# Kernel optimization log

Measured on AMD Instinct MI355X. Metric: run time of the kernel, lower is better.

## Reference

```python
import jax, jax.numpy as jnp
import numpy as np

D_INP=36; D_MODEL=144; NHEAD=4; NHID=128; NLAYERS=2
MAX_LEN=215; D_STATIC=9; D_PE=16; N_CLASSES=2; B=128
D_OB=D_MODEL//D_INP; GCH=MAX_LEN*D_OB; D_TR=D_MODEL+D_PE; D_FINAL=D_TR+D_INP
_EI=np.stack(np.nonzero(np.ones((D_INP,D_INP),dtype=np.int64)))  # torch.nonzero(ones).T -> all pairs
SRC_N=jnp.asarray(_EI[0]); TGT_N=jnp.asarray(_EI[1]); N_EDGE=_EI.shape[1]


def setup_inputs():
    ks=jax.random.split(jax.random.key(0),40)
    def w(i,shape,s=0.05): return jax.random.normal(ks[i],shape,jnp.float32)*s
    return {
      'src': jax.random.normal(ks[0],(MAX_LEN,B,2*D_INP),jnp.float32),
      'static': jax.random.normal(ks[1],(B,D_STATIC),jnp.float32),
      'times': jax.random.uniform(ks[2],(MAX_LEN,B),jnp.float32)*MAX_LEN,
      'lengths': jax.random.randint(ks[3],(B,),32,MAX_LEN+1),
      'R_u': w(4,(1,D_INP*D_OB)),
      'emb_w': w(5,(D_INP,D_STATIC)), 'emb_b': jnp.zeros(D_INP,jnp.float32),
      'Wv1': w(6,(GCH,GCH),1.0/np.sqrt(GCH)), 'bv1': jnp.zeros(GCH,jnp.float32),
      'Wv2': w(7,(GCH,GCH),1.0/np.sqrt(GCH)), 'bv2': jnp.zeros(GCH,jnp.float32),
      'in_proj_w': w(8,(NLAYERS,3*D_TR,D_TR)), 'in_proj_b': jnp.zeros((NLAYERS,3*D_TR),jnp.float32),
      'out_w': w(9,(NLAYERS,D_TR,D_TR)), 'out_b': jnp.zeros((NLAYERS,D_TR),jnp.float32),
      'lin1_w': w(10,(NLAYERS,NHID,D_TR)), 'lin1_b': jnp.zeros((NLAYERS,NHID),jnp.float32),
      'lin2_w': w(11,(NLAYERS,D_TR,NHID)), 'lin2_b': jnp.zeros((NLAYERS,D_TR),jnp.float32),
      'ln1_s': jnp.ones((NLAYERS,D_TR),jnp.float32), 'ln1_b': jnp.zeros((NLAYERS,D_TR),jnp.float32),
      'ln2_s': jnp.ones((NLAYERS,D_TR),jnp.float32), 'ln2_b': jnp.zeros((NLAYERS,D_TR),jnp.float32),
      'mlp1_w': w(12,(D_FINAL,D_FINAL)), 'mlp1_b': jnp.zeros(D_FINAL,jnp.float32),
      'mlp2_w': w(13,(N_CLASSES,D_FINAL)), 'mlp2_b': jnp.zeros(N_CLASSES,jnp.float32),
    }


def _seg_softmax(wgt, seg, n):
    m=jnp.full((n,),-jnp.inf,wgt.dtype).at[seg].max(wgt)
    e=jnp.exp(wgt-m[seg])
    s=jnp.zeros((n,),wgt.dtype).at[seg].add(e)
    return e/s[seg]


def _ln(x,s,b):
    mu=jnp.mean(x,-1,keepdims=True); v=jnp.var(x,-1,keepdims=True)
    return (x-mu)/jnp.sqrt(v+1e-5)*s+b


def _forward(src, static, times, R_u, emb_w, emb_b, Wv1, bv1, Wv2, bv2, in_proj_w, in_proj_b, out_w, out_b, lin1_w, lin1_b, lin2_w, lin2_b, ln1_s, ln1_b, ln2_s, ln2_b, mlp1_w, mlp1_b, mlp2_w, mlp2_b, lengths):
    T,Bb=src.shape[0],src.shape[1]
    obs=src[:,:,:D_INP]                                  # drop mask half
    h=jax.nn.relu(jnp.repeat(obs,D_OB,axis=-1)*R_u)      # h_u = relu(x_u*R_u), [T,B,144]
    ts=jnp.asarray(MAX_LEN**np.linspace(0,1,D_PE//2),jnp.float32)
    scaled=times[:,:,None]/ts
    pe=jnp.concatenate([jnp.sin(scaled),jnp.cos(scaled)],-1)  # [T,B,16]
    emb=static@emb_w.T+emb_b                             # [B,36]
    # --- Observation_progation x2 (use_beta=False): gather-softmax-scatter per sensor graph ---
    xb=h.transpose(1,0,2).reshape(Bb,T,D_INP,D_OB).transpose(0,2,1,3).reshape(Bb,D_INP,GCH)
    ew=jnp.ones((N_EDGE,),jnp.float32)                   # adj=ones -> edge_weights=1
    gamma=_seg_softmax(ew,TGT_N,D_INP)                   # softmax over edges per target node
    def prop(x_,Wv,bv):
        V=jax.nn.relu(x_@Wv.T+bv)                        # relu(lin_value(x_j))
        msgs=V[:,SRC_N,:]*gamma[None,:,None]             # gather source features per edge
        return jnp.zeros_like(x_).at[:,TGT_N,:].add(msgs)  # scatter-add to targets
    x1=prop(xb,Wv1,bv1)
    x2=prop(x1,Wv2,bv2)                                  # layer2 uses alpha1 = raw edge_weights
    alpha=jnp.broadcast_to(ew[None,:],(Bb,N_EDGE))       # alpha_all.T
    sq=jnp.sum(alpha*alpha,1)
    d2=jnp.maximum(sq[:,None]+sq[None,:]-2.0*(alpha@alpha.T),0.0)
    distance=jnp.mean(jnp.sqrt(d2))
    out=x2.reshape(Bb,D_INP,T,D_OB).transpose(2,0,1,3).reshape(T,Bb,D_INP*D_OB)
    x=jnp.concatenate([out,pe],-1)                       # [T,B,160]
    mask=jnp.arange(T)[None,:]>=lengths[:,None]          # [B,T] True = padded
    hd=D_TR//NHEAD
    for l in range(NLAYERS):                             # torch post-norm TransformerEncoderLayer
        qkv=x@in_proj_w[l].T+in_proj_b[l]
        q,k,v=jnp.split(qkv,3,-1)
        def heads(t): return t.reshape(T,Bb,NHEAD,hd).transpose(1,2,0,3)  # [B,H,T,hd]
        sc=jnp.einsum('bhqd,bhkd->bhqk',heads(q),heads(k))/np.sqrt(hd)
        sc=jnp.where(mask[:,None,None,:],jnp.float32(-1e30),sc)
        o=jnp.einsum('bhqk,bhkd->bhqd',jax.nn.softmax(sc,-1),heads(v))
        o=o.transpose(2,0,1,3).reshape(T,Bb,D_TR)@out_w[l].T+out_b[l]
        x=_ln(x+o,ln1_s[l],ln1_b[l])
        ff=jax.nn.relu(x@lin1_w[l].T+lin1_b[l])@lin2_w[l].T+lin2_b[l]
        x=_ln(x+ff,ln2_s[l],ln2_b[l])
    valid=1.0-mask.T[:,:,None].astype(x.dtype)           # [T,B,1]
    agg=jnp.sum(x*valid,0)/(lengths[:,None].astype(x.dtype)+1.0)
    feat=jnp.concatenate([agg,emb],1)                    # [B,196]
    logits=jax.nn.relu(feat@mlp1_w.T+mlp1_b)@mlp2_w.T+mlp2_b
    return logits,distance


def reference(src, static, times, lengths, R_u, emb_w, emb_b, Wv1, bv1, Wv2, bv2, in_proj_w, in_proj_b, out_w, out_b, lin1_w, lin1_b, lin2_w, lin2_b, ln1_s, ln1_b, ln2_s, ln2_b, mlp1_w, mlp1_b, mlp2_w, mlp2_b):
    return _forward(src, static, times, R_u, emb_w, emb_b, Wv1, bv1, Wv2, bv2, in_proj_w, in_proj_b, out_w, out_b, lin1_w, lin1_b, lin2_w, lin2_b, ln1_s, ln1_b, ln2_s, ln2_b, mlp1_w, mlp1_b, mlp2_w, mlp2_b, lengths)
```

## Files before the change

kernel.cpp:

```cpp
#include <hip/hip_runtime.h>
#include <math.h>

#define T_LEN 215
#define TP    224
#define B_N   128
#define DINP  36
#define D_TR  160
#define HD    40
#define D_FIN 196
#define KPG   864

typedef __attribute__((ext_vector_type(8))) short short8v;
typedef __attribute__((ext_vector_type(4))) float f32x4;

__device__ __forceinline__ ushort f2bf(float x) {
  union { float f; unsigned u; } c; c.f = x;
  unsigned r = c.u + 0x7fffu + ((c.u >> 16) & 1u);
  return (ushort)(r >> 16);
}
__device__ __forceinline__ float bf2f(ushort h) {
  union { unsigned u; float f; } c; c.u = ((unsigned)h) << 16;
  return c.f;
}

__global__ __launch_bounds__(256) void k_prep(const float* __restrict__ Wv1,
    const float* __restrict__ Wv2, const float* __restrict__ ipw, const float* __restrict__ ow,
    const float* __restrict__ l1w, const float* __restrict__ l2w,
    const float* __restrict__ src, const float* __restrict__ R_u,
    const float* __restrict__ stat, const float* __restrict__ emb_w, const float* __restrict__ emb_b,
    ushort* __restrict__ wv1b, ushort* __restrict__ wv2b, ushort* __restrict__ ipwb,
    ushort* __restrict__ owb, ushort* __restrict__ l1wb, ushort* __restrict__ l2wb,
    float* __restrict__ v2acc, float* __restrict__ featacc,
    ushort* __restrict__ obuf16, ushort* __restrict__ xb16) {
  __shared__ float Ss[T_LEN * DINP];
  if (blockIdx.x >= 8202) {
    const int b = blockIdx.x - 8202, tid = threadIdx.x;
    for (int i = tid; i < T_LEN * DINP; i += 256) {
      int t = i / DINP, j = i - t * DINP;
      Ss[i] = src[((size_t)t * B_N + b) * 72 + j];
    }
    __syncthreads();
    for (int i = tid; i < DINP * T_LEN; i += 256) {
      int ii = i / T_LEN, t = i - ii * T_LEN;
      float v = Ss[t * DINP + ii];
      float4 r = ((const float4*)R_u)[ii];
      ushort4 o;
      o.x = f2bf(fmaxf(v * r.x, 0.f)); o.y = f2bf(fmaxf(v * r.y, 0.f));
      o.z = f2bf(fmaxf(v * r.z, 0.f)); o.w = f2bf(fmaxf(v * r.w, 0.f));
      ushort* row = xb16 + (size_t)(b * DINP + ii) * KPG;
      *(ushort4*)(row + 4 * t) = o;
      if (t == 0) { ushort4 z = {0, 0, 0, 0}; *(ushort4*)(row + 860) = z; }
    }
    return;
  }
  int i = blockIdx.x * 256 + threadIdx.x;
  if (i < 746496) { int n = i / KPG, k = i % KPG;
    wv1b[i] = (n < 860 && k < 860) ? f2bf(Wv1[n * 860 + k]) : (ushort)0; return; }
  i -= 746496;
  if (i < 746496) { int n = i / KPG, k = i % KPG;
    wv2b[i] = (n < 860 && k < 860) ? f2bf(Wv2[n * 860 + k]) : (ushort)0; return; }
  i -= 746496;
  if (i < 153600) { ipwb[i] = f2bf(ipw[i]); return; }
  i -= 153600;
  if (i < 51200)  { owb[i] = f2bf(ow[i]); return; }
  i -= 51200;
  if (i < 40960)  { l1wb[i] = f2bf(l1w[i]); return; }
  i -= 40960;
  if (i < 40960)  { l2wb[i] = f2bf(l2w[i]); return; }
  i -= 40960;
  if (i < 110592) { v2acc[i] = 0.f; return; }
  i -= 110592;
  if (i < 20480)  { int b = i / D_TR, d = i - b * D_TR;
    featacc[b * D_FIN + d] = 0.f; return; }
  i -= 20480;
  if (i < 4608)   { int b = i / DINP, ii = i - b * DINP;
    float s = emb_b[ii];
    #pragma unroll
    for (int k = 0; k < 9; k++) s = fmaf(stat[b * 9 + k], emb_w[ii * 9 + k], s);
    featacc[b * D_FIN + D_TR + ii] = s; return; }
  i -= 4608;
  if (i < 184320) {
    int b = i / 1440, rem = i % 1440;
    int t = 215 + rem / 160, cc = rem % 160;
    obuf16[((size_t)b * TP + t) * D_TR + cc] = 0; return;
  }
}

__global__ __launch_bounds__(256) void k_red_s1(const ushort* __restrict__ V1b, ushort* __restrict__ s1) {
  int idx = blockIdx.x * 256 + threadIdx.x;
  if (idx >= B_N * KPG) return;
  int b = idx / KPG, n = idx % KPG;
  float s = 0.f;
  if (n < 860) {
    #pragma unroll 4
    for (int i = 0; i < DINP; i++) s += bf2f(V1b[((size_t)b * DINP + i) * 860 + n]);
    s *= (1.0f / 36.0f);
  }
  s1[idx] = (n < 860) ? f2bf(s) : (ushort)0;
}

__global__ __launch_bounds__(256) void k_buildx(const float* __restrict__ v2acc,
    const float* __restrict__ bv2, const float* __restrict__ times,
    ushort* __restrict__ x16) {
  int idx = blockIdx.x * 256 + threadIdx.x;
  if (idx >= B_N * TP * 40) return;
  int c = idx % 40;
  int r = idx / 40;
  int t = r % TP, b = r / TP;
  float4 f = {0.f, 0.f, 0.f, 0.f};
  if (t < T_LEN) {
    if (c < 36) {
      float4 a = *(const float4*)&v2acc[(size_t)b * KPG + 4 * t];
      float4 bb = *(const float4*)&bv2[4 * t];
      f.x = fmaxf(a.x + bb.x, 0.f); f.y = fmaxf(a.y + bb.y, 0.f);
      f.z = fmaxf(a.z + bb.z, 0.f); f.w = fmaxf(a.w + bb.w, 0.f);
    } else {
      float tm = times[t * B_N + b];
      int j0 = (c - 36) * 4;
      bool is_sin = j0 < 8;
      int kb = j0 & 7;
      float o[4];
      #pragma unroll
      for (int qq = 0; qq < 4; qq++) {
        float ts = expf((float)(kb + qq) * 0.76723400f);
        float sc = tm / ts;
        o[qq] = is_sin ? sinf(sc) : cosf(sc);
      }
      f.x = o[0]; f.y = o[1]; f.z = o[2]; f.w = o[3];
    }
  }
  ushort4 h = {f2bf(f.x), f2bf(f.y), f2bf(f.z), f2bf(f.w)};
  *(ushort4*)(x16 + (size_t)r * D_TR + 4 * c) = h;
}

template <int RELU, int SPLIT, int WMODE, int BNT>
__global__ __launch_bounds__(256) void gemm_bf16(const ushort* __restrict__ A,
    const ushort* __restrict__ W, const float* __restrict__ bias, void* __restrict__ Cv,
    int KP, int ldc, int ncols, int kts) {
  __shared__ ushort As[128 * 32];
  __shared__ ushort Ws[BNT * 32];
  constexpr int NJ = BNT / 16;
  const int tid = threadIdx.x;
  const int wave = tid >> 6, lane = tid & 63;
  const int lr = lane & 15, hi = lane >> 4;
  const int m0 = blockIdx.y * 128, n0 = blockIdx.x * BNT;
  const int kt0 = blockIdx.z * kts;

  f32x4 acc[2][NJ];
  #pragma unroll
  for (int i = 0; i < 2; i++)
    #pragma unroll
    for (int j = 0; j < NJ; j++) acc[i][j] = (f32x4){0.f, 0.f, 0.f, 0.f};

  const int ar = tid >> 2, g = tid & 3;
  const size_t abase0 = (size_t)(m0 + ar) * KP;
  const size_t abase1 = (size_t)(m0 + ar + 64) * KP;
  const size_t bbase0 = (size_t)(n0 + ar) * KP;
  const size_t bbase1 = (size_t)(n0 + ar + 64) * KP;
  const int awb0 = ar * 64 + ((g * 16) ^ ((ar & 3) << 4));
  const int awb1 = awb0 + 64 * 64;

  const int arow0 = wave * 32 + lr;
  const int arb0 = arow0 * 64 + ((hi * 16) ^ ((arow0 & 3) << 4));
  const int arb1 = (arow0 + 16) * 64 + ((hi * 16) ^ (((arow0 + 16) & 3) << 4));
  int brb[NJ];
  #pragma unroll
  for (int j = 0; j < NJ; j++)
    brb[j] = (j * 16 + lr) * 64 + ((hi * 16) ^ ((lr & 3) << 4));

  for (int kt = 0; kt < kts; ++kt) {
    const int k0 = (kt0 + kt) * 32;
    uint4 va0 = *(const uint4*)(A + abase0 + k0 + g * 8);
    uint4 va1 = *(const uint4*)(A + abase1 + k0 + g * 8);
    uint4 vb0 = *(const uint4*)(W + bbase0 + k0 + g * 8);
    uint4 vb1;
    if constexpr (BNT == 128) vb1 = *(const uint4*)(W + bbase1 + k0 + g * 8);
    if (kt) __syncthreads();
    *(uint4*)((char*)As + awb0) = va0;
    *(uint4*)((char*)As + awb1) = va1;
    *(uint4*)((char*)Ws + awb0) = vb0;
    if constexpr (BNT == 128) *(uint4*)((char*)Ws + awb1) = vb1;
    __syncthreads();
    short8v a0 = *(const short8v*)((const char*)As + arb0);
    short8v a1 = *(const short8v*)((const char*)As + arb1);
    #pragma unroll
    for (int j = 0; j < NJ; j++) {
      short8v bf = *(const short8v*)((const char*)Ws + brb[j]);
      acc[0][j] = __builtin_amdgcn_mfma_f32_16x16x32_bf16(a0, bf, acc[0][j], 0, 0, 0);
      acc[1][j] = __builtin_amdgcn_mfma_f32_16x16x32_bf16(a1, bf, acc[1][j], 0, 0, 0);
    }
  }

  #pragma unroll
  for (int i = 0; i < 2; i++) {
    #pragma unroll
    for (int j = 0; j < NJ; j++) {
      int col = n0 + j * 16 + lr;
      int row = m0 + wave * 32 + i * 16 + hi * 4;
      if (col < ncols) {
        if constexpr (SPLIT) {
          #pragma unroll
          for (int r = 0; r < 4; r++)
            atomicAdd((float*)Cv + (size_t)(row + r) * ldc + col, acc[i][j][r]);
        } else {
          float bb = bias ? bias[col] : 0.f;
          #pragma unroll
          for (int r = 0; r < 4; r++) {
            float xv = acc[i][j][r] + bb;
            if (RELU) xv = fmaxf(xv, 0.f);
            if (WMODE == 0) ((float*)Cv)[(size_t)(row + r) * ldc + col] = xv;
            else            ((ushort*)Cv)[(size_t)(row + r) * ldc + col] = f2bf(xv);
          }
        }
      }
    }
  }
}

__global__ __launch_bounds__(256) void gemm_qkv(const ushort* __restrict__ A,
    const ushort* __restrict__ W, const float* __restrict__ bias,
    ushort* __restrict__ qkvB, ushort* __restrict__ Vt, int kts) {
  __shared__ ushort As[128 * 32];
  __shared__ ushort Ws[128 * 32];
  const int KP = 160;
  const int tid = threadIdx.x;
  const int wave = tid >> 6, lane = tid & 63;
  const int lr = lane & 15, hi = lane >> 4;
  const int m0 = blockIdx.y * 128, n0 = blockIdx.x * 128;

  f32x4 acc[2][8];
  #pragma unroll
  for (int i = 0; i < 2; i++)
    #pragma unroll
    for (int j = 0; j < 8; j++) acc[i][j] = (f32x4){0.f, 0.f, 0.f, 0.f};

  const int ar = tid >> 2, g = tid & 3;
  const size_t abase0 = (size_t)(m0 + ar) * KP;
  const size_t abase1 = (size_t)(m0 + ar + 64) * KP;
  const size_t bbase0 = (size_t)(n0 + ar) * KP;
  const size_t bbase1 = (size_t)(n0 + ar + 64) * KP;
  const int awb0 = ar * 64 + ((g * 16) ^ ((ar & 3) << 4));
  const int awb1 = awb0 + 64 * 64;

  const int arow0 = wave * 32 + lr;
  const int arb0 = arow0 * 64 + ((hi * 16) ^ ((arow0 & 3) << 4));
  const int arb1 = (arow0 + 16) * 64 + ((hi * 16) ^ (((arow0 + 16) & 3) << 4));
  int brb[8];
  #pragma unroll
  for (int j = 0; j < 8; j++)
    brb[j] = (j * 16 + lr) * 64 + ((hi * 16) ^ ((lr & 3) << 4));

  for (int kt = 0; kt < kts; ++kt) {
    const int k0 = kt * 32;
    uint4 va0 = *(const uint4*)(A + abase0 + k0 + g * 8);
    uint4 va1 = *(const uint4*)(A + abase1 + k0 + g * 8);
    uint4 vb0 = *(const uint4*)(W + bbase0 + k0 + g * 8);
    uint4 vb1 = *(const uint4*)(W + bbase1 + k0 + g * 8);
    if (kt) __syncthreads();
    *(uint4*)((char*)As + awb0) = va0;
    *(uint4*)((char*)As + awb1) = va1;
    *(uint4*)((char*)Ws + awb0) = vb0;
    *(uint4*)((char*)Ws + awb1) = vb1;
    __syncthreads();
    short8v a0 = *(const short8v*)((const char*)As + arb0);
    short8v a1 = *(const short8v*)((const char*)As + arb1);
    #pragma unroll
    for (int j = 0; j < 8; j++) {
      short8v bf = *(const short8v*)((const char*)Ws + brb[j]);
      acc[0][j] = __builtin_amdgcn_mfma_f32_16x16x32_bf16(a0, bf, acc[0][j], 0, 0, 0);
      acc[1][j] = __builtin_amdgcn_mfma_f32_16x16x32_bf16(a1, bf, acc[1][j], 0, 0, 0);
    }
  }

  #pragma unroll
  for (int i = 0; i < 2; i++) {
    const int row = m0 + wave * 32 + i * 16 + hi * 4;
    const int b = row / TP, t0 = row - b * TP;
    #pragma unroll
    for (int j = 0; j < 8; j++) {
      int col = n0 + j * 16 + lr;
      if (col < 320) {
        float bb = bias[col];
        #pragma unroll
        for (int r = 0; r < 4; r++)
          qkvB[(size_t)(row + r) * 480 + col] = f2bf(acc[i][j][r] + bb);
      } else if (col < 480) {
        float bb = bias[col];
        int dg = col - 320;
        int hh = dg / 40, dd = dg - hh * 40;
        ushort4 pv;
        pv.x = f2bf(acc[i][j][0] + bb); pv.y = f2bf(acc[i][j][1] + bb);
        pv.z = f2bf(acc[i][j][2] + bb); pv.w = f2bf(acc[i][j][3] + bb);
        *(ushort4*)(Vt + (((size_t)(b * 4 + hh) * 48 + dd) * TP + t0)) = pv;
      }
    }
  }
}

__global__ __launch_bounds__(256) void gemm_ln(const ushort* __restrict__ A,
    const ushort* __restrict__ W, const float* __restrict__ bias,
    const float* __restrict__ gam, const float* __restrict__ bet,
    ushort* __restrict__ x16, int KP, int kts,
    const int* __restrict__ lengths, float* __restrict__ featacc) {
  __shared__ ushort As[64 * 32];
  __shared__ ushort Ws[160 * 32];
  const int tid = threadIdx.x;
  const int wave = tid >> 6, lane = tid & 63;
  const int lr = lane & 15, hi = lane >> 4;
  const int m0 = blockIdx.x * 64;

  f32x4 acc[10];
  #pragma unroll
  for (int j = 0; j < 10; j++) acc[j] = (f32x4){0.f, 0.f, 0.f, 0.f};

  const int ar = tid >> 2, g = tid & 3;
  const size_t abase = (size_t)(m0 + ar) * KP;
  const int awb = ar * 64 + ((g * 16) ^ ((ar & 3) << 4));
  const int wr0 = tid >> 2,         ws0 = tid & 3;
  const int wr1 = (tid + 256) >> 2, ws1 = (tid + 256) & 3;
  const int wr2 = (tid + 512) >> 2, ws2 = (tid + 512) & 3;
  const int wwb0 = wr0 * 64 + ((ws0 * 16) ^ ((wr0 & 3) << 4));
  const int wwb1 = wr1 * 64 + ((ws1 * 16) ^ ((wr1 & 3) << 4));
  const int wwb2 = wr2 * 64 + ((ws2 * 16) ^ ((wr2 & 3) << 4));

  const int arow = wave * 16 + lr;
  const int arb = arow * 64 + ((hi * 16) ^ ((arow & 3) << 4));
  int brb[10];
  #pragma unroll
  for (int j = 0; j < 10; j++)
    brb[j] = (j * 16 + lr) * 64 + ((hi * 16) ^ ((lr & 3) << 4));

  for (int kt = 0; kt < kts; ++kt) {
    const int k0 = kt * 32;
    uint4 va = *(const uint4*)(A + abase + k0 + g * 8);
    uint4 w0 = *(const uint4*)(W + (size_t)wr0 * KP + k0 + ws0 * 8);
    uint4 w1 = *(const uint4*)(W + (size_t)wr1 * KP + k0 + ws1 * 8);
    uint4 w2;
    if (tid < 128) w2 = *(const uint4*)(W + (size_t)wr2 * KP + k0 + ws2 * 8);
    if (kt) __syncthreads();
    *(uint4*)((char*)As + awb) = va;
    *(uint4*)((char*)Ws + wwb0) = w0;
    *(uint4*)((char*)Ws + wwb1) = w1;
    if (tid < 128) *(uint4*)((char*)Ws + wwb2) = w2;
    __syncthreads();
    short8v a0 = *(const short8v*)((const char*)As + arb);
    #pragma unroll
    for (int j = 0; j < 10; j++) {
      short8v bf = *(const short8v*)((const char*)Ws + brb[j]);
      acc[j] = __builtin_amdgcn_mfma_f32_16x16x32_bf16(a0, bf, acc[j], 0, 0, 0);
    }
  }

  const int rb = m0 + wave * 16 + hi * 4;
  float s[4] = {0.f, 0.f, 0.f, 0.f};
  #pragma unroll
  for (int j = 0; j < 10; j++) {
    const int col = j * 16 + lr;
    const float bb = bias[col];
    #pragma unroll
    for (int r = 0; r < 4; r++) {
      float v = acc[j][r] + bb + bf2f(x16[(size_t)(rb + r) * D_TR + col]);
      acc[j][r] = v;
      s[r] += v;
    }
  }
  #pragma unroll
  for (int r = 0; r < 4; r++) {
    s[r] += __shfl_xor(s[r], 1, 64);
    s[r] += __shfl_xor(s[r], 2, 64);
    s[r] += __shfl_xor(s[r], 4, 64);
    s[r] += __shfl_xor(s[r], 8, 64);
  }
  float mu[4], q2[4] = {0.f, 0.f, 0.f, 0.f};
  #pragma unroll
  for (int r = 0; r < 4; r++) mu[r] = s[r] * (1.0f / 160.0f);
  #pragma unroll
  for (int j = 0; j < 10; j++)
    #pragma unroll
    for (int r = 0; r < 4; r++) {
      float d = acc[j][r] - mu[r];
      q2[r] += d * d;
    }
  #pragma unroll
  for (int r = 0; r < 4; r++) {
    q2[r] += __shfl_xor(q2[r], 1, 64);
    q2[r] += __shfl_xor(q2[r], 2, 64);
    q2[r] += __shfl_xor(q2[r], 4, 64);
    q2[r] += __shfl_xor(q2[r], 8, 64);
  }
  float rstd[4];
  #pragma unroll
  for (int r = 0; r < 4; r++) rstd[r] = rsqrtf(q2[r] * (1.0f / 160.0f) + 1e-5f);

  if (featacc == nullptr) {
    #pragma unroll
    for (int j = 0; j < 10; j++) {
      const int col = j * 16 + lr;
      const float gc = gam[col], bc = bet[col];
      #pragma unroll
      for (int r = 0; r < 4; r++) {
        float o = (acc[j][r] - mu[r]) * rstd[r] * gc + bc;
        x16[(size_t)(rb + r) * D_TR + col] = f2bf(o);
      }
    }
  } else {
    const int b = rb / TP, t0 = rb - b * TP;
    int L = lengths[b]; if (L > T_LEN) L = T_LEN;
    #pragma unroll
    for (int j = 0; j < 10; j++) {
      const int col = j * 16 + lr;
      const float gc = gam[col], bc = bet[col];
      float sacc = 0.f;
      #pragma unroll
      for (int r = 0; r < 4; r++) {
        float o = (acc[j][r] - mu[r]) * rstd[r] * gc + bc;
        if (t0 + r < L) sacc += o;
      }
      if (t0 < L) atomicAdd(&featacc[b * D_FIN + col], sacc);
    }
  }
}

__global__ __launch_bounds__(256) void gemm_ff(const ushort* __restrict__ x16in,
    const ushort* __restrict__ W1, const float* __restrict__ b1,
    const ushort* __restrict__ W2, const float* __restrict__ b2,
    const float* __restrict__ gam, const float* __restrict__ bet,
    ushort* __restrict__ x16, const int* __restrict__ lengths,
    float* __restrict__ featacc) {
  __shared__ ushort As[64 * 32];
  __shared__ ushort W1s[128 * 32];
  __shared__ ushort W2s[160 * 32];
  __shared__ ushort Hs[64 * 136];
  const int tid = threadIdx.x;
  const int wave = tid >> 6, lane = tid & 63;
  const int lr = lane & 15, hi = lane >> 4;
  const int m0 = blockIdx.x * 64;

  f32x4 acc1[8];
  #pragma unroll
  for (int j = 0; j < 8; j++) acc1[j] = (f32x4){0.f, 0.f, 0.f, 0.f};

  const int ar = tid >> 2, g = tid & 3;
  const size_t abase = (size_t)(m0 + ar) * 160;
  const int awb = ar * 64 + ((g * 16) ^ ((ar & 3) << 4));
  const int awb1 = awb + 64 * 64;
  const size_t w1base0 = (size_t)ar * 160;
  const size_t w1base1 = (size_t)(ar + 64) * 160;

  const int arow = wave * 16 + lr;
  const int arb = arow * 64 + ((hi * 16) ^ ((arow & 3) << 4));
  int brb8[8];
  #pragma unroll
  for (int j = 0; j < 8; j++)
    brb8[j] = (j * 16 + lr) * 64 + ((hi * 16) ^ ((lr & 3) << 4));

  for (int kt = 0; kt < 5; ++kt) {
    const int k0 = kt * 32;
    uint4 va  = *(const uint4*)(x16in + abase + k0 + g * 8);
    uint4 w10 = *(const uint4*)(W1 + w1base0 + k0 + g * 8);
    uint4 w11 = *(const uint4*)(W1 + w1base1 + k0 + g * 8);
    if (kt) __syncthreads();
    *(uint4*)((char*)As + awb) = va;
    *(uint4*)((char*)W1s + awb) = w10;
    *(uint4*)((char*)W1s + awb1) = w11;
    __syncthreads();
    short8v a0 = *(const short8v*)((const char*)As + arb);
    #pragma unroll
    for (int j = 0; j < 8; j++) {
      short8v bf = *(const short8v*)((const char*)W1s + brb8[j]);
      acc1[j] = __builtin_amdgcn_mfma_f32_16x16x32_bf16(a0, bf, acc1[j], 0, 0, 0);
    }
  }
  {
    const int rr = wave * 16 + hi * 4;
    #pragma unroll
    for (int j = 0; j < 8; j++) {
      const int col = j * 16 + lr;
      const float bb = b1[col];
      #pragma unroll
      for (int r = 0; r < 4; r++)
        Hs[(rr + r) * 136 + col] = f2bf(fmaxf(acc1[j][r] + bb, 0.f));
    }
  }
  __syncthreads();

  f32x4 acc[10];
  #pragma unroll
  for (int j = 0; j < 10; j++) acc[j] = (f32x4){0.f, 0.f, 0.f, 0.f};

  const int wr0 = tid >> 2,         ws0 = tid & 3;
  const int wr1 = (tid + 256) >> 2, ws1 = (tid + 256) & 3;
  const int wr2 = (tid + 512) >> 2, ws2 = (tid + 512) & 3;
  const int wwb0 = wr0 * 64 + ((ws0 * 16) ^ ((wr0 & 3) << 4));
  const int wwb1 = wr1 * 64 + ((ws1 * 16) ^ ((wr1 & 3) << 4));
  const int wwb2 = wr2 * 64 + ((ws2 * 16) ^ ((wr2 & 3) << 4));
  int brb[10];
  #pragma unroll
  for (int j = 0; j < 10; j++)
    brb[j] = (j * 16 + lr) * 64 + ((hi * 16) ^ ((lr & 3) << 4));

  for (int kt = 0; kt < 4; ++kt) {
    const int k0 = kt * 32;
    uint4 w0 = *(const uint4*)(W2 + (size_t)wr0 * 128 + k0 + ws0 * 8);
    uint4 w1 = *(const uint4*)(W2 + (size_t)wr1 * 128 + k0 + ws1 * 8);
    uint4 w2;
    if (tid < 128) w2 = *(const uint4*)(W2 + (size_t)wr2 * 128 + k0 + ws2 * 8);
    if (kt) __syncthreads();
    *(uint4*)((char*)W2s + wwb0) = w0;
    *(uint4*)((char*)W2s + wwb1) = w1;
    if (tid < 128) *(uint4*)((char*)W2s + wwb2) = w2;
    __syncthreads();
    short8v a0 = *(const short8v*)(&Hs[(wave * 16 + lr) * 136 + k0 + hi * 8]);
    #pragma unroll
    for (int j = 0; j < 10; j++) {
      short8v bf = *(const short8v*)((const char*)W2s + brb[j]);
      acc[j] = __builtin_amdgcn_mfma_f32_16x16x32_bf16(a0, bf, acc[j], 0, 0, 0);
    }
  }

  const int rb = m0 + wave * 16 + hi * 4;
  float s[4] = {0.f, 0.f, 0.f, 0.f};
  #pragma unroll
  for (int j = 0; j < 10; j++) {
    const int col = j * 16 + lr;
    const float bb = b2[col];
    #pragma unroll
    for (int r = 0; r < 4; r++) {
      float v = acc[j][r] + bb + bf2f(x16[(size_t)(rb + r) * D_TR + col]);
      acc[j][r] = v;
      s[r] += v;
    }
  }
  #pragma unroll
  for (int r = 0; r < 4; r++) {
    s[r] += __shfl_xor(s[r], 1, 64);
    s[r] += __shfl_xor(s[r], 2, 64);
    s[r] += __shfl_xor(s[r], 4, 64);
    s[r] += __shfl_xor(s[r], 8, 64);
  }
  float mu[4], q2[4] = {0.f, 0.f, 0.f, 0.f};
  #pragma unroll
  for (int r = 0; r < 4; r++) mu[r] = s[r] * (1.0f / 160.0f);
  #pragma unroll
  for (int j = 0; j < 10; j++)
    #pragma unroll
    for (int r = 0; r < 4; r++) {
      float d = acc[j][r] - mu[r];
      q2[r] += d * d;
    }
  #pragma unroll
  for (int r = 0; r < 4; r++) {
    q2[r] += __shfl_xor(q2[r], 1, 64);
    q2[r] += __shfl_xor(q2[r], 2, 64);
    q2[r] += __shfl_xor(q2[r], 4, 64);
    q2[r] += __shfl_xor(q2[r], 8, 64);
  }
  float rstd[4];
  #pragma unroll
  for (int r = 0; r < 4; r++) rstd[r] = rsqrtf(q2[r] * (1.0f / 160.0f) + 1e-5f);

  if (featacc == nullptr) {
    #pragma unroll
    for (int j = 0; j < 10; j++) {
      const int col = j * 16 + lr;
      const float gc = gam[col], bc = bet[col];
      #pragma unroll
      for (int r = 0; r < 4; r++) {
        float o = (acc[j][r] - mu[r]) * rstd[r] * gc + bc;
        x16[(size_t)(rb + r) * D_TR + col] = f2bf(o);
      }
    }
  } else {
    const int b = rb / TP, t0 = rb - b * TP;
    int L = lengths[b]; if (L > T_LEN) L = T_LEN;
    #pragma unroll
    for (int j = 0; j < 10; j++) {
      const int col = j * 16 + lr;
      const float gc = gam[col], bc = bet[col];
      float sacc = 0.f;
      #pragma unroll
      for (int r = 0; r < 4; r++) {
        float o = (acc[j][r] - mu[r]) * rstd[r] * gc + bc;
        if (t0 + r < L) sacc += o;
      }
      if (t0 < L) atomicAdd(&featacc[b * D_FIN + col], sacc);
    }
  }
}

__global__ __launch_bounds__(64) void k_attn4(const ushort* __restrict__ qkvB,
    const ushort* __restrict__ Vt, const int* __restrict__ lengths,
    ushort* __restrict__ o16) {
  __shared__ ushort SP[16 * 232];
  const int bh = blockIdx.x;
  const int b = bh >> 2, h = bh & 3;
  int L = lengths[b]; if (L > T_LEN) L = T_LEN;
  const int q0 = blockIdx.y << 4;
  if (q0 >= L) return;
  const int lane = threadIdx.x;
  const int lr = lane & 15, hi = lane >> 4;
  const int nk16 = (L + 15) >> 4;
  const int nkt  = (L + 31) >> 5;
  const float SC = 0.15811388300841898f;

  const ushort* qrow = qkvB + ((size_t)b * TP + q0) * 480 + h * 40;
  uint4 qa0u = *(const uint4*)(qrow + lr * 480 + hi * 8);
  uint4 qa1u = {0, 0, 0, 0};
  if (hi == 0) qa1u = *(const uint4*)(qrow + lr * 480 + 32);
  short8v qa0 = *(short8v*)&qa0u;
  short8v qa1 = *(short8v*)&qa1u;

  f32x4 c[14];
  #pragma unroll
  for (int kt = 0; kt < 14; ++kt) {
    c[kt] = (f32x4){0.f, 0.f, 0.f, 0.f};
    if (kt < nk16) {
      const ushort* krow = qkvB + ((size_t)b * TP + kt * 16) * 480 + 160 + h * 40;
      uint4 kb0u = *(const uint4*)(krow + lr * 480 + hi * 8);
      uint4 kb1u = {0, 0, 0, 0};
      if (hi == 0) kb1u = *(const uint4*)(krow + lr * 480 + 32);
      c[kt] = __builtin_amdgcn_mfma_f32_16x16x32_bf16(qa0, *(short8v*)&kb0u, c[kt], 0, 0, 0);
      c[kt] = __builtin_amdgcn_mfma_f32_16x16x32_bf16(qa1, *(short8v*)&kb1u, c[kt], 0, 0, 0);
    }
  }

  float mx[4] = {-1e30f, -1e30f, -1e30f, -1e30f};
  #pragma unroll
  for (int kt = 0; kt < 14; ++kt) {
    if (kt < nk16) {
      bool valid = (kt * 16 + lr) < L;
      #pragma unroll
      for (int r = 0; r < 4; r++) {
        float v = valid ? c[kt][r] : -1e30f;
        mx[r] = fmaxf(mx[r], v);
      }
    }
  }
  #pragma unroll
  for (int r = 0; r < 4; r++) {
    mx[r] = fmaxf(mx[r], __shfl_xor(mx[r], 1, 64));
    mx[r] = fmaxf(mx[r], __shfl_xor(mx[r], 2, 64));
    mx[r] = fmaxf(mx[r], __shfl_xor(mx[r], 4, 64));
    mx[r] = fmaxf(mx[r], __shfl_xor(mx[r], 8, 64));
  }
  float sum[4] = {0.f, 0.f, 0.f, 0.f};
  #pragma unroll
  for (int kt = 0; kt < 14; ++kt) {
    if (kt < nk16) {
      bool valid = (kt * 16 + lr) < L;
      #pragma unroll
      for (int r = 0; r < 4; r++) {
        float p = valid ? __expf(SC * (c[kt][r] - mx[r])) : 0.f;
        sum[r] += p;
        c[kt][r] = p;
      }
    }
  }
  #pragma unroll
  for (int r = 0; r < 4; r++) {
    sum[r] += __shfl_xor(sum[r], 1, 64);
    sum[r] += __shfl_xor(sum[r], 2, 64);
    sum[r] += __shfl_xor(sum[r], 4, 64);
    sum[r] += __shfl_xor(sum[r], 8, 64);
  }

  const int nk16w = nkt * 2;
  #pragma unroll
  for (int kt = 0; kt < 14; ++kt) {
    if (kt < nk16w) {
      #pragma unroll
      for (int r = 0; r < 4; r++)
        SP[(hi * 4 + r) * 232 + kt * 16 + lr] = f2bf(c[kt][r]);
    }
  }
  __syncthreads();

  f32x4 o0 = {0.f, 0.f, 0.f, 0.f}, o1 = o0, o2 = o0;
  const ushort* vbase = Vt + (size_t)bh * 48 * TP;
  #pragma unroll
  for (int kt = 0; kt < 7; ++kt) {
    if (kt < nkt) {
      short8v pa = *(const short8v*)((const char*)SP + lr * 464 + kt * 64 + hi * 16);
      const ushort* vb = vbase + kt * 32 + hi * 8;
      short8v v0 = *(const short8v*)(vb + (size_t)lr * TP);
      short8v v1 = *(const short8v*)(vb + (size_t)(16 + lr) * TP);
      short8v v2 = *(const short8v*)(vb + (size_t)(32 + lr) * TP);
      o0 = __builtin_amdgcn_mfma_f32_16x16x32_bf16(pa, v0, o0, 0, 0, 0);
      o1 = __builtin_amdgcn_mfma_f32_16x16x32_bf16(pa, v1, o1, 0, 0, 0);
      o2 = __builtin_amdgcn_mfma_f32_16x16x32_bf16(pa, v2, o2, 0, 0, 0);
    }
  }

  #pragma unroll
  for (int r = 0; r < 4; r++) {
    int t = q0 + hi * 4 + r;
    if (t < T_LEN) {
      float inv = 1.0f / sum[r];
      ushort* op = o16 + ((size_t)b * TP + t) * D_TR + h * 40;
      op[lr]      = f2bf(o0[r] * inv);
      op[16 + lr] = f2bf(o1[r] * inv);
      if (lr < 8) op[32 + lr] = f2bf(o2[r] * inv);
    }
  }
}

__global__ __launch_bounds__(256) void k_head2(const float* __restrict__ featacc,
    const int* __restrict__ lengths, const float* __restrict__ m1w,
    const float* __restrict__ m1b, const float* __restrict__ m2w,
    const float* __restrict__ m2b, float* __restrict__ out) {
  __shared__ float feat[196];
  __shared__ float m1o_s[196];
  __shared__ float r0[4], r1[4];
  const int b = blockIdx.x, tid = threadIdx.x;
  int L = lengths[b]; if (L > T_LEN) L = T_LEN;
  const float inv = 1.0f / (float)(L + 1);
  if (tid < D_FIN)
    feat[tid] = featacc[(size_t)b * D_FIN + tid] * (tid < D_TR ? inv : 1.f);
  __syncthreads();
  if (tid < D_FIN) {
    float s = m1b[tid];
    const float* wr = m1w + (size_t)tid * D_FIN;
    #pragma unroll 4
    for (int k = 0; k < D_FIN; k++) s = fmaf(feat[k], wr[k], s);
    m1o_s[tid] = fmaxf(s, 0.f);
  }
  __syncthreads();
  float p0 = 0.f, p1 = 0.f;
  if (tid < D_FIN) {
    p0 = m1o_s[tid] * m2w[tid];
    p1 = m1o_s[tid] * m2w[D_FIN + tid];
  }
  #pragma unroll
  for (int off = 32; off; off >>= 1) {
    p0 += __shfl_xor(p0, off, 64);
    p1 += __shfl_xor(p1, off, 64);
  }
  int w = tid >> 6;
  if ((tid & 63) == 0) { r0[w] = p0; r1[w] = p1; }
  __syncthreads();
  if (tid == 0) out[2 * b]     = r0[0] + r0[1] + r0[2] + r0[3] + m2b[0];
  if (tid == 1) out[2 * b + 1] = r1[0] + r1[1] + r1[2] + r1[3] + m2b[1];
  if (b == 0 && tid == 2) out[256] = 0.f;
}

extern "C" void kernel_launch(void* const* d_in, const int* in_sizes, int n_in,
                              void* d_out, int out_size, void* d_ws, size_t ws_size,
                              hipStream_t stream) {
  const float* src   = (const float*)d_in[0];
  const float* stat  = (const float*)d_in[1];
  const float* times = (const float*)d_in[2];
  const int*   lens  = (const int*)d_in[3];
  const float* R_u   = (const float*)d_in[4];
  const float* emb_w = (const float*)d_in[5];
  const float* emb_b = (const float*)d_in[6];
  const float* Wv1   = (const float*)d_in[7];
  const float* bv1   = (const float*)d_in[8];
  const float* Wv2   = (const float*)d_in[9];
  const float* bv2   = (const float*)d_in[10];
  const float* ipw   = (const float*)d_in[11];
  const float* ipb   = (const float*)d_in[12];
  const float* ow    = (const float*)d_in[13];
  const float* ob    = (const float*)d_in[14];
  const float* l1w   = (const float*)d_in[15];
  const float* l1b   = (const float*)d_in[16];
  const float* l2w   = (const float*)d_in[17];
  const float* l2b   = (const float*)d_in[18];
  const float* ln1s  = (const float*)d_in[19];
  const float* ln1bb = (const float*)d_in[20];
  const float* ln2s  = (const float*)d_in[21];
  const float* ln2bb = (const float*)d_in[22];
  const float* m1w   = (const float*)d_in[23];
  const float* m1b   = (const float*)d_in[24];
  const float* m2w   = (const float*)d_in[25];
  const float* m2b   = (const float*)d_in[26];
  float* out = (float*)d_out;

  char* p = (char*)d_ws;
  ushort* x16    = (ushort*)p;  p += 9175040;
  float*  v2acc  = (float*)p;   p += 442368;
  ushort* s1b    = (ushort*)p;  p += 221184;
  ushort* obuf16 = (ushort*)p;  p += 9175040;
  ushort* wv1b   = (ushort*)p;  p += 1492992;
  ushort* wv2b   = (ushort*)p;  p += 1492992;
  ushort* ipwb   = (ushort*)p;  p += 307200;
  ushort* owb    = (ushort*)p;  p += 102400;
  ushort* l1wb   = (ushort*)p;  p += 81920;
  ushort* l2wb   = (ushort*)p;  p += 81920;
  float*  featacc= (float*)p;   p += 100352;
  char*   R2     = p;
  ushort* xb16   = (ushort*)R2;
  ushort* V1b    = (ushort*)(R2 + 7962624);
  ushort* qkvB   = (ushort*)R2;
  ushort* Vt     = (ushort*)(R2 + 27525120);

  k_prep<<<8330, 256, 0, stream>>>(Wv1, Wv2, ipw, ow, l1w, l2w, src, R_u,
                                   stat, emb_w, emb_b,
                                   wv1b, wv2b, ipwb, owb, l1wb, l2wb,
                                   v2acc, featacc, obuf16, xb16);

  gemm_bf16<1, 0, 1, 128><<<dim3(7, 36, 1), 256, 0, stream>>>(
      xb16, wv1b, bv1, V1b, KPG, 860, 860, 27);
  k_red_s1<<<432, 256, 0, stream>>>(V1b, s1b);
  gemm_bf16<0, 1, 0, 64><<<dim3(14, 1, 9), 256, 0, stream>>>(
      s1b, wv2b, nullptr, v2acc, KPG, KPG, KPG, 3);
  k_buildx<<<4480, 256, 0, stream>>>(v2acc, bv2, times, x16);

  for (int l = 0; l < 2; l++) {
    gemm_qkv<<<dim3(4, 224, 1), 256, 0, stream>>>(
        x16, ipwb + (size_t)l * 76800, ipb + l * 480, qkvB, Vt, 5);
    k_attn4<<<dim3(512, 14), 64, 0, stream>>>(qkvB, Vt, lens, obuf16);
    gemm_ln<<<448, 256, 0, stream>>>(obuf16, owb + (size_t)l * 25600, ob + l * 160,
                                     ln1s + l * 160, ln1bb + l * 160, x16, 160, 5,
                                     lens, nullptr);
    gemm_ff<<<448, 256, 0, stream>>>(x16, l1wb + (size_t)l * 20480, l1b + l * 128,
                                     l2wb + (size_t)l * 20480, l2b + l * 160,
                                     ln2s + l * 160, ln2bb + l * 160, x16, lens,
                                     (l == 1) ? featacc : nullptr);
  }

  k_head2<<<128, 256, 0, stream>>>(featacc, lens, m1w, m1b, m2w, m2b, out);
}
```

Baseline: 233.7 us.

## Fuse out-projection+LN1 with feed-forward+LN2 into one kernel

```diff
diff --git a/kernel.cpp b/kernel.cpp
--- a/kernel.cpp
+++ b/kernel.cpp
@@ -297,32 +297,34 @@
   }
 }
 
-__global__ __launch_bounds__(256) void gemm_ln(const ushort* __restrict__ A,
-    const ushort* __restrict__ W, const float* __restrict__ bias,
-    const float* __restrict__ gam, const float* __restrict__ bet,
-    ushort* __restrict__ x16, int KP, int kts,
-    const int* __restrict__ lengths, float* __restrict__ featacc) {
+__global__ __launch_bounds__(256) void gemm_lnff(const ushort* __restrict__ Ao,
+    const ushort* __restrict__ Wo, const float* __restrict__ bo,
+    const float* __restrict__ g1, const float* __restrict__ be1,
+    const ushort* __restrict__ W1, const float* __restrict__ b1,
+    const ushort* __restrict__ W2, const float* __restrict__ b2,
+    const float* __restrict__ g2, const float* __restrict__ be2,
+    ushort* __restrict__ x16, const int* __restrict__ lengths,
+    float* __restrict__ featacc) {
   __shared__ ushort As[64 * 32];
   __shared__ ushort Ws[160 * 32];
+  __shared__ ushort W1s[128 * 32];
+  __shared__ ushort W2s[160 * 32];
+  __shared__ ushort Xln[64 * 168];
+  __shared__ ushort Hs[64 * 136];
   const int tid = threadIdx.x;
   const int wave = tid >> 6, lane = tid & 63;
   const int lr = lane & 15, hi = lane >> 4;
   const int m0 = blockIdx.x * 64;
 
-  f32x4 acc[10];
-  #pragma unroll
-  for (int j = 0; j < 10; j++) acc[j] = (f32x4){0.f, 0.f, 0.f, 0.f};
-
   const int ar = tid >> 2, g = tid & 3;
-  const size_t abase = (size_t)(m0 + ar) * KP;
   const int awb = ar * 64 + ((g * 16) ^ ((ar & 3) << 4));
+  const int awb1 = awb + 64 * 64;
   const int wr0 = tid >> 2,         ws0 = tid & 3;
   const int wr1 = (tid + 256) >> 2, ws1 = (tid + 256) & 3;
   const int wr2 = (tid + 512) >> 2, ws2 = (tid + 512) & 3;
   const int wwb0 = wr0 * 64 + ((ws0 * 16) ^ ((wr0 & 3) << 4));
   const int wwb1 = wr1 * 64 + ((ws1 * 16) ^ ((wr1 & 3) << 4));
   const int wwb2 = wr2 * 64 + ((ws2 * 16) ^ ((wr2 & 3) << 4));
-
   const int arow = wave * 16 + lr;
   const int arb = arow * 64 + ((hi * 16) ^ ((arow & 3) << 4));
   int brb[10];
@@ -330,260 +332,208 @@
   for (int j = 0; j < 10; j++)
     brb[j] = (j * 16 + lr) * 64 + ((hi * 16) ^ ((lr & 3) << 4));
 
-  for (int kt = 0; kt < kts; ++kt) {
-    const int k0 = kt * 32;
-    uint4 va = *(const uint4*)(A + abase + k0 + g * 8);
-    uint4 w0 = *(const uint4*)(W + (size_t)wr0 * KP + k0 + ws0 * 8);
-    uint4 w1 = *(const uint4*)(W + (size_t)wr1 * KP + k0 + ws1 * 8);
-    uint4 w2;
-    if (tid < 128) w2 = *(const uint4*)(W + (size_t)wr2 * KP + k0 + ws2 * 8);
-    if (kt) __syncthreads();
-    *(uint4*)((char*)As + awb) = va;
-    *(uint4*)((char*)Ws + wwb0) = w0;
-    *(uint4*)((char*)Ws + wwb1) = w1;
-    if (tid < 128) *(uint4*)((char*)Ws + wwb2) = w2;
-    __syncthreads();
-    short8v a0 = *(const short8v*)((const char*)As + arb);
-    #pragma unroll
-    for (int j = 0; j < 10; j++) {
-      short8v bf = *(const short8v*)((const char*)Ws + brb[j]);
-      acc[j] = __builtin_amdgcn_mfma_f32_16x16x32_bf16(a0, bf, acc[j], 0, 0, 0);
-    }
-  }
-
-  const int rb = m0 + wave * 16 + hi * 4;
-  float s[4] = {0.f, 0.f, 0.f, 0.f};
-  #pragma unroll
-  for (int j = 0; j < 10; j++) {
-    const int col = j * 16 + lr;
-    const float bb = bias[col];
-    #pragma unroll
-    for (int r = 0; r < 4; r++) {
-      float v = acc[j][r] + bb + bf2f(x16[(size_t)(rb + r) * D_TR + col]);
-      acc[j][r] = v;
-      s[r] += v;
-    }
-  }
-  #pragma unroll
-  for (int r = 0; r < 4; r++) {
-    s[r] += __shfl_xor(s[r], 1, 64);
-    s[r] += __shfl_xor(s[r], 2, 64);
-    s[r] += __shfl_xor(s[r], 4, 64);
-    s[r] += __shfl_xor(s[r], 8, 64);
-  }
-  float mu[4], q2[4] = {0.f, 0.f, 0.f, 0.f};
-  #pragma unroll
-  for (int r = 0; r < 4; r++) mu[r] = s[r] * (1.0f / 160.0f);
-  #pragma unroll
-  for (int j = 0; j < 10; j++)
-    #pragma unroll
-    for (int r = 0; r < 4; r++) {
-      float d = acc[j][r] - mu[r];
-      q2[r] += d * d;
-    }
-  #pragma unroll
-  for (int r = 0; r < 4; r++) {
-    q2[r] += __shfl_xor(q2[r], 1, 64);
-    q2[r] += __shfl_xor(q2[r], 2, 64);
-    q2[r] += __shfl_xor(q2[r], 4, 64);
-    q2[r] += __shfl_xor(q2[r], 8, 64);
-  }
-  float rstd[4];
-  #pragma unroll
-  for (int r = 0; r < 4; r++) rstd[r] = rsqrtf(q2[r] * (1.0f / 160.0f) + 1e-5f);
-
-  if (featacc == nullptr) {
+  const int lrow0 = wave * 16 + hi * 4;
+  const int rb = m0 + lrow0;
+
+  {
+    f32x4 acc[10];
+    #pragma unroll
+    for (int j = 0; j < 10; j++) acc[j] = (f32x4){0.f, 0.f, 0.f, 0.f};
+    const size_t abase = (size_t)(m0 + ar) * 160;
+    for (int kt = 0; kt < 5; ++kt) {
+      const int k0 = kt * 32;
+      uint4 va = *(const uint4*)(Ao + abase + k0 + g * 8);
+      uint4 w0 = *(const uint4*)(Wo + (size_t)wr0 * 160 + k0 + ws0 * 8);
+      uint4 w1 = *(const uint4*)(Wo + (size_t)wr1 * 160 + k0 + ws1 * 8);
+      uint4 w2;
+      if (tid < 128) w2 = *(const uint4*)(Wo + (size_t)wr2 * 160 + k0 + ws2 * 8);
+      if (kt) __syncthreads();
+      *(uint4*)((char*)As + awb) = va;
+      *(uint4*)((char*)Ws + wwb0) = w0;
+      *(uint4*)((char*)Ws + wwb1) = w1;
+      if (tid < 128) *(uint4*)((char*)Ws + wwb2) = w2;
+      __syncthreads();
+      short8v a0 = *(const short8v*)((const char*)As + arb);
+      #pragma unroll
+      for (int j = 0; j < 10; j++) {
+        short8v bf = *(const short8v*)((const char*)Ws + brb[j]);
+        acc[j] = __builtin_amdgcn_mfma_f32_16x16x32_bf16(a0, bf, acc[j], 0, 0, 0);
+      }
+    }
+    float s[4] = {0.f, 0.f, 0.f, 0.f};
     #pragma unroll
     for (int j = 0; j < 10; j++) {
       const int col = j * 16 + lr;
-      const float gc = gam[col], bc = bet[col];
+      const float bb = bo[col];
+      #pragma unroll
+      for (int r = 0; r < 4; r++) {
+        float v = acc[j][r] + bb + bf2f(x16[(size_t)(rb + r) * D_TR + col]);
+        acc[j][r] = v;
+        s[r] += v;
+      }
+    }
+    #pragma unroll
+    for (int r = 0; r < 4; r++) {
+      s[r] += __shfl_xor(s[r], 1, 64);
+      s[r] += __shfl_xor(s[r], 2, 64);
+      s[r] += __shfl_xor(s[r], 4, 64);
+      s[r] += __shfl_xor(s[r], 8, 64);
+    }
+    float mu[4], q2[4] = {0.f, 0.f, 0.f, 0.f};
+    #pragma unroll
+    for (int r = 0; r < 4; r++) mu[r] = s[r] * (1.0f / 160.0f);
+    #pragma unroll
+    for (int j = 0; j < 10; j++)
+      #pragma unroll
+      for (int r = 0; r < 4; r++) {
+        float d = acc[j][r] - mu[r];
+        q2[r] += d * d;
+      }
+    #pragma unroll
+    for (int r = 0; r < 4; r++) {
+      q2[r] += __shfl_xor(q2[r], 1, 64);
+      q2[r] += __shfl_xor(q2[r], 2, 64);
+      q2[r] += __shfl_xor(q2[r], 4, 64);
+      q2[r] += __shfl_xor(q2[r], 8, 64);
+    }
+    float rstd[4];
+    #pragma unroll
+    for (int r = 0; r < 4; r++) rstd[r] = rsqrtf(q2[r] * (1.0f / 160.0f) + 1e-5f);
+    #pragma unroll
+    for (int j = 0; j < 10; j++) {
+      const int col = j * 16 + lr;
+      const float gc = g1[col], bc = be1[col];
       #pragma unroll
       for (int r = 0; r < 4; r++) {
         float o = (acc[j][r] - mu[r]) * rstd[r] * gc + bc;
-        x16[(size_t)(rb + r) * D_TR + col] = f2bf(o);
-      }
-    }
-  } else {
-    const int b = rb / TP, t0 = rb - b * TP;
-    int L = lengths[b]; if (L > T_LEN) L = T_LEN;
-    #pragma unroll
-    for (int j = 0; j < 10; j++) {
-      const int col = j * 16 + lr;
-      const float gc = gam[col], bc = bet[col];
-      float sacc = 0.f;
-      #pragma unroll
-      for (int r = 0; r < 4; r++) {
-        float o = (acc[j][r] - mu[r]) * rstd[r] * gc + bc;
-        if (t0 + r < L) sacc += o;
-      }
-      if (t0 < L) atomicAdd(&featacc[b * D_FIN + col], sacc);
-    }
-  }
-}
-
-__global__ __launch_bounds__(256) void gemm_ff(const ushort* __restrict__ x16in,
-    const ushort* __restrict__ W1, const float* __restrict__ b1,
-    const ushort* __restrict__ W2, const float* __restrict__ b2,
-    const float* __restrict__ gam, const float* __restrict__ bet,
-    ushort* __restrict__ x16, const int* __restrict__ lengths,
-    float* __restrict__ featacc) {
-  __shared__ ushort As[64 * 32];
-  __shared__ ushort W1s[128 * 32];
-  __shared__ ushort W2s[160 * 32];
-  __shared__ ushort Hs[64 * 136];
-  const int tid = threadIdx.x;
-  const int wave = tid >> 6, lane = tid & 63;
-  const int lr = lane & 15, hi = lane >> 4;
-  const int m0 = blockIdx.x * 64;
-
-  f32x4 acc1[8];
-  #pragma unroll
-  for (int j = 0; j < 8; j++) acc1[j] = (f32x4){0.f, 0.f, 0.f, 0.f};
-
-  const int ar = tid >> 2, g = tid & 3;
-  const size_t abase = (size_t)(m0 + ar) * 160;
-  const int awb = ar * 64 + ((g * 16) ^ ((ar & 3) << 4));
-  const int awb1 = awb + 64 * 64;
-  const size_t w1base0 = (size_t)ar * 160;
-  const size_t w1base1 = (size_t)(ar + 64) * 160;
-
-  const int arow = wave * 16 + lr;
-  const int arb = arow * 64 + ((hi * 16) ^ ((arow & 3) << 4));
-  int brb8[8];
-  #pragma unroll
-  for (int j = 0; j < 8; j++)
-    brb8[j] = (j * 16 + lr) * 64 + ((hi * 16) ^ ((lr & 3) << 4));
-
-  for (int kt = 0; kt < 5; ++kt) {
-    const int k0 = kt * 32;
-    uint4 va  = *(const uint4*)(x16in + abase + k0 + g * 8);
-    uint4 w10 = *(const uint4*)(W1 + w1base0 + k0 + g * 8);
-    uint4 w11 = *(const uint4*)(W1 + w1base1 + k0 + g * 8);
-    if (kt) __syncthreads();
-    *(uint4*)((char*)As + awb) = va;
-    *(uint4*)((char*)W1s + awb) = w10;
-    *(uint4*)((char*)W1s + awb1) = w11;
-    __syncthreads();
-    short8v a0 = *(const short8v*)((const char*)As + arb);
-    #pragma unroll
-    for (int j = 0; j < 8; j++) {
-      short8v bf = *(const short8v*)((const char*)W1s + brb8[j]);
-      acc1[j] = __builtin_amdgcn_mfma_f32_16x16x32_bf16(a0, bf, acc1[j], 0, 0, 0);
-    }
-  }
+        Xln[(lrow0 + r) * 168 + col] = f2bf(o);
+      }
+    }
+  }
+  __syncthreads();
+
   {
-    const int rr = wave * 16 + hi * 4;
+    f32x4 acc1[8];
+    #pragma unroll
+    for (int j = 0; j < 8; j++) acc1[j] = (f32x4){0.f, 0.f, 0.f, 0.f};
+    int brb8[8];
+    #pragma unroll
+    for (int j = 0; j < 8; j++)
+      brb8[j] = (j * 16 + lr) * 64 + ((hi * 16) ^ ((lr & 3) << 4));
+    for (int kt = 0; kt < 5; ++kt) {
+      const int k0 = kt * 32;
+      uint4 w10 = *(const uint4*)(W1 + (size_t)ar * 160 + k0 + g * 8);
+      uint4 w11 = *(const uint4*)(W1 + (size_t)(ar + 64) * 160 + k0 + g * 8);
+      if (kt) __syncthreads();
+      *(uint4*)((char*)W1s + awb) = w10;
+      *(uint4*)((char*)W1s + awb1) = w11;
+      __syncthreads();
+      short8v a0 = *(const short8v*)(&Xln[(wave * 16 + lr) * 168 + k0 + hi * 8]);
+      #pragma unroll
+      for (int j = 0; j < 8; j++) {
+        short8v bf = *(const short8v*)((const char*)W1s + brb8[j]);
+        acc1[j] = __builtin_amdgcn_mfma_f32_16x16x32_bf16(a0, bf, acc1[j], 0, 0, 0);
+      }
+    }
     #pragma unroll
     for (int j = 0; j < 8; j++) {
       const int col = j * 16 + lr;
       const float bb = b1[col];
       #pragma unroll
       for (int r = 0; r < 4; r++)
-        Hs[(rr + r) * 136 + col] = f2bf(fmaxf(acc1[j][r] + bb, 0.f));
+        Hs[(lrow0 + r) * 136 + col] = f2bf(fmaxf(acc1[j][r] + bb, 0.f));
     }
   }
   __syncthreads();
 
-  f32x4 acc[10];
-  #pragma unroll
-  for (int j = 0; j < 10; j++) acc[j] = (f32x4){0.f, 0.f, 0.f, 0.f};
-
-  const int wr0 = tid >> 2,         ws0 = tid & 3;
-  const int wr1 = (tid + 256) >> 2, ws1 = (tid + 256) & 3;
-  const int wr2 = (tid + 512) >> 2, ws2 = (tid + 512) & 3;
-  const int wwb0 = wr0 * 64 + ((ws0 * 16) ^ ((wr0 & 3) << 4));
-  const int wwb1 = wr1 * 64 + ((ws1 * 16) ^ ((wr1 & 3) << 4));
-  const int wwb2 = wr2 * 64 + ((ws2 * 16) ^ ((wr2 & 3) << 4));
-  int brb[10];
-  #pragma unroll
-  for (int j = 0; j < 10; j++)
-    brb[j] = (j * 16 + lr) * 64 + ((hi * 16) ^ ((lr & 3) << 4));
-
-  for (int kt = 0; kt < 4; ++kt) {
-    const int k0 = kt * 32;
-    uint4 w0 = *(const uint4*)(W2 + (size_t)wr0 * 128 + k0 + ws0 * 8);
-    uint4 w1 = *(const uint4*)(W2 + (size_t)wr1 * 128 + k0 + ws1 * 8);
-    uint4 w2;
-    if (tid < 128) w2 = *(const uint4*)(W2 + (size_t)wr2 * 128 + k0 + ws2 * 8);
-    if (kt) __syncthreads();
-    *(uint4*)((char*)W2s + wwb0) = w0;
-    *(uint4*)((char*)W2s + wwb1) = w1;
-    if (tid < 128) *(uint4*)((char*)W2s + wwb2) = w2;
-    __syncthreads();
-    short8v a0 = *(const short8v*)(&Hs[(wave * 16 + lr) * 136 + k0 + hi * 8]);
-    #pragma unroll
-    for (int j = 0; j < 10; j++) {
-      short8v bf = *(const short8v*)((const char*)W2s + brb[j]);
-      acc[j] = __builtin_amdgcn_mfma_f32_16x16x32_bf16(a0, bf, acc[j], 0, 0, 0);
-    }
-  }
-
-  const int rb = m0 + wave * 16 + hi * 4;
-  float s[4] = {0.f, 0.f, 0.f, 0.f};
-  #pragma unroll
-  for (int j = 0; j < 10; j++) {
-    const int col = j * 16 + lr;
-    const float bb = b2[col];
-    #pragma unroll
-    for (int r = 0; r < 4; r++) {
-      float v = acc[j][r] + bb + bf2f(x16[(size_t)(rb + r) * D_TR + col]);
-      acc[j][r] = v;
-      s[r] += v;
-    }
-  }
-  #pragma unroll
-  for (int r = 0; r < 4; r++) {
-    s[r] += __shfl_xor(s[r], 1, 64);
-    s[r] += __shfl_xor(s[r], 2, 64);
-    s[r] += __shfl_xor(s[r], 4, 64);
-    s[r] += __shfl_xor(s[r], 8, 64);
-  }
-  float mu[4], q2[4] = {0.f, 0.f, 0.f, 0.f};
-  #pragma unroll
-  for (int r = 0; r < 4; r++) mu[r] = s[r] * (1.0f / 160.0f);
-  #pragma unroll
-  for (int j = 0; j < 10; j++)
-    #pragma unroll
-    for (int r = 0; r < 4; r++) {
-      float d = acc[j][r] - mu[r];
-      q2[r] += d * d;
-    }
-  #pragma unroll
-  for (int r = 0; r < 4; r++) {
-    q2[r] += __shfl_xor(q2[r], 1, 64);
-    q2[r] += __shfl_xor(q2[r], 2, 64);
-    q2[r] += __shfl_xor(q2[r], 4, 64);
-    q2[r] += __shfl_xor(q2[r], 8, 64);
-  }
-  float rstd[4];
-  #pragma unroll
-  for (int r = 0; r < 4; r++) rstd[r] = rsqrtf(q2[r] * (1.0f / 160.0f) + 1e-5f);
-
-  if (featacc == nullptr) {
+  {
+    f32x4 acc[10];
+    #pragma unroll
+    for (int j = 0; j < 10; j++) acc[j] = (f32x4){0.f, 0.f, 0.f, 0.f};
+    for (int kt = 0; kt < 4; ++kt) {
+      const int k0 = kt * 32;
+      uint4 w0 = *(const uint4*)(W2 + (size_t)wr0 * 128 + k0 + ws0 * 8);
+      uint4 w1 = *(const uint4*)(W2 + (size_t)wr1 * 128 + k0 + ws1 * 8);
+      uint4 w2;
+      if (tid < 128) w2 = *(const uint4*)(W2 + (size_t)wr2 * 128 + k0 + ws2 * 8);
+      if (kt) __syncthreads();
+      *(uint4*)((char*)W2s + wwb0) = w0;
+      *(uint4*)((char*)W2s + wwb1) = w1;
+      if (tid < 128) *(uint4*)((char*)W2s + wwb2) = w2;
+      __syncthreads();
+      short8v a0 = *(const short8v*)(&Hs[(wave * 16 + lr) * 136 + k0 + hi * 8]);
+      #pragma unroll
+      for (int j = 0; j < 10; j++) {
+        short8v bf = *(const short8v*)((const char*)W2s + brb[j]);
+        acc[j] = __builtin_amdgcn_mfma_f32_16x16x32_bf16(a0, bf, acc[j], 0, 0, 0);
+      }
+    }
+    float s[4] = {0.f, 0.f, 0.f, 0.f};
     #pragma unroll
     for (int j = 0; j < 10; j++) {
       const int col = j * 16 + lr;
-      const float gc = gam[col], bc = bet[col];
+      const float bb = b2[col];
       #pragma unroll
       for (int r = 0; r < 4; r++) {
-        float o = (acc[j][r] - mu[r]) * rstd[r] * gc + bc;
-        x16[(size_t)(rb + r) * D_TR + col] = f2bf(o);
-      }
-    }
-  } else {
-    const int b = rb / TP, t0 = rb - b * TP;
-    int L = lengths[b]; if (L > T_LEN) L = T_LEN;
-    #pragma unroll
-    for (int j = 0; j < 10; j++) {
-      const int col = j * 16 + lr;
-      const float gc = gam[col], bc = bet[col];
-      float sacc = 0.f;
+        float v = acc[j][r] + bb + bf2f(Xln[(lrow0 + r) * 168 + col]);
+        acc[j][r] = v;
+        s[r] += v;
+      }
+    }
+    #pragma unroll
+    for (int r = 0; r < 4; r++) {
+      s[r] += __shfl_xor(s[r], 1, 64);
+      s[r] += __shfl_xor(s[r], 2, 64);
+      s[r] += __shfl_xor(s[r], 4, 64);
+      s[r] += __shfl_xor(s[r], 8, 64);
+    }
+    float mu[4], q2[4] = {0.f, 0.f, 0.f, 0.f};
+    #pragma unroll
+    for (int r = 0; r < 4; r++) mu[r] = s[r] * (1.0f / 160.0f);
+    #pragma unroll
+    for (int j = 0; j < 10; j++)
       #pragma unroll
       for (int r = 0; r < 4; r++) {
-        float o = (acc[j][r] - mu[r]) * rstd[r] * gc + bc;
-        if (t0 + r < L) sacc += o;
-      }
-      if (t0 < L) atomicAdd(&featacc[b * D_FIN + col], sacc);
+        float d = acc[j][r] - mu[r];
+        q2[r] += d * d;
+      }
+    #pragma unroll
+    for (int r = 0; r < 4; r++) {
+      q2[r] += __shfl_xor(q2[r], 1, 64);
+      q2[r] += __shfl_xor(q2[r], 2, 64);
+      q2[r] += __shfl_xor(q2[r], 4, 64);
+      q2[r] += __shfl_xor(q2[r], 8, 64);
+    }
+    float rstd[4];
+    #pragma unroll
+    for (int r = 0; r < 4; r++) rstd[r] = rsqrtf(q2[r] * (1.0f / 160.0f) + 1e-5f);
+
+    if (featacc == nullptr) {
+      #pragma unroll
+      for (int j = 0; j < 10; j++) {
+        const int col = j * 16 + lr;
+        const float gc = g2[col], bc = be2[col];
+        #pragma unroll
+        for (int r = 0; r < 4; r++) {
+          float o = (acc[j][r] - mu[r]) * rstd[r] * gc + bc;
+          x16[(size_t)(rb + r) * D_TR + col] = f2bf(o);
+        }
+      }
+    } else {
+      const int b = rb / TP, t0 = rb - b * TP;
+      int L = lengths[b]; if (L > T_LEN) L = T_LEN;
+      #pragma unroll
+      for (int j = 0; j < 10; j++) {
+        const int col = j * 16 + lr;
+        const float gc = g2[col], bc = be2[col];
+        float sacc = 0.f;
+        #pragma unroll
+        for (int r = 0; r < 4; r++) {
+          float o = (acc[j][r] - mu[r]) * rstd[r] * gc + bc;
+          if (t0 + r < L) sacc += o;
+        }
+        if (t0 < L) atomicAdd(&featacc[b * D_FIN + col], sacc);
+      }
     }
   }
 }
@@ -809,13 +759,13 @@
     gemm_qkv<<<dim3(4, 224, 1), 256, 0, stream>>>(
         x16, ipwb + (size_t)l * 76800, ipb + l * 480, qkvB, Vt, 5);
     k_attn4<<<dim3(512, 14), 64, 0, stream>>>(qkvB, Vt, lens, obuf16);
-    gemm_ln<<<448, 256, 0, stream>>>(obuf16, owb + (size_t)l * 25600, ob + l * 160,
-                                     ln1s + l * 160, ln1bb + l * 160, x16, 160, 5,
-                                     lens, nullptr);
-    gemm_ff<<<448, 256, 0, stream>>>(x16, l1wb + (size_t)l * 20480, l1b + l * 128,
-                                     l2wb + (size_t)l * 20480, l2b + l * 160,
-                                     ln2s + l * 160, ln2bb + l * 160, x16, lens,
-                                     (l == 1) ? featacc : nullptr);
+    gemm_lnff<<<448, 256, 0, stream>>>(
+        obuf16, owb + (size_t)l * 25600, ob + l * 160,
+        ln1s + l * 160, ln1bb + l * 160,
+        l1wb + (size_t)l * 20480, l1b + l * 128,
+        l2wb + (size_t)l * 20480, l2b + l * 160,
+        ln2s + l * 160, ln2bb + l * 160,
+        x16, lens, (l == 1) ? featacc : nullptr);
   }
 
   k_head2<<<128, 256, 0, stream>>>(featacc, lens, m1w, m1b, m2w, m2b, out);
```

Result: faster. 225.4 us (median of 2 runs) (-3.5%).
